# Kernel optimization log

Hardware: AMD Instinct MI355X
Metric: run time of the kernel (lower is better)

The kernel has to match this reference:

```python
import jax, jax.numpy as jnp
import numpy as np

N = 4096          # total atoms
N_METAL = 1024    # first N_METAL atoms are metal (Z=79) by construction
L = 24.0          # cubic cell edge (Angstrom)
DL = 2.4
NK = 10           # int(L / DL) -- static k-grid extent per axis
SIGMA = 1.0 / 1.805132
SCALING = 1.0
FOUR_PI = 4.0 * np.pi

# static integer reciprocal grid with k=0 removed: (K,3), K = (2*NK+1)^3 - 1
_g = np.arange(-NK, NK + 1)
_INTS = np.stack(np.meshgrid(_g, _g, _g, indexing="ij"), axis=-1).reshape(-1, 3)
_INTS = _INTS[np.any(_INTS != 0, axis=1)].astype(np.float32)


def _ewald_potential(r, q, cell):
    """Reciprocal-space Ewald potential at each atom position.
    r: (n,3) positions, q: (n,m) charges (m charge columns), cell: (3,3)
    rows = lattice vectors. Returns (n,m) potential ('field' f in cace).
    pot_i = (4*pi/V) * sum_k exp(-sigma^2 k^2/2)/k^2 * Re[S(k) e^{-ik.r_i}]."""
    recip = (2.0 * np.pi) * jnp.linalg.inv(cell).T      # rows b1,b2,b3
    k = jnp.asarray(_INTS, dtype=r.dtype) @ recip       # (K,3)
    k2 = jnp.sum(k * k, axis=1)                         # (K,)
    kfac = jnp.exp((-0.5 * SIGMA * SIGMA) * k2) / k2    # (K,)
    vol = jnp.abs(jnp.linalg.det(cell))
    kr = r @ k.T                                        # (n,K)  dominant alloc
    c, s = jnp.cos(kr), jnp.sin(kr)
    sf_c = c.T @ q                                      # (K,m) structure factors
    sf_s = s.T @ q
    pot = c @ (kfac[:, None] * sf_c) + s @ (kfac[:, None] * sf_s)
    return (FOUR_PI / vol) * pot


def setup_inputs() -> dict:
    key = jax.random.key(0)
    k1, k2 = jax.random.split(key)
    positions = jax.random.uniform(k1, (N, 3), dtype=jnp.float32) * L
    q = jax.random.normal(k2, (N, 1), dtype=jnp.float32) * 0.1
    cell = (L * jnp.eye(3, dtype=jnp.float32)).reshape(1, 3, 3)
    atomic_numbers = jnp.concatenate([
        jnp.full((N_METAL,), 79, dtype=jnp.int32),   # metal block first
        jnp.full((N - N_METAL,), 8, dtype=jnp.int32),
    ])
    batch = jnp.zeros((N,), dtype=jnp.int32)         # single system
    return {"positions": positions, "q": q, "cell": cell,
            "atomic_numbers": atomic_numbers, "batch": batch}


def reference(positions, q, cell, atomic_numbers, batch):
    # single batch (batch all zeros); metal atoms are the first N_METAL
    # (atomic_numbers == 79 by construction, so the boolean mask is static)
    cell0 = cell.reshape(3, 3)
    q = q.at[:N_METAL].set(0.0)                      # q_all[metal] = 0
    r_m = positions[:N_METAL]

    # _compute_S_matrix: pairwise Ewald kernel among metal atoms via q=eye
    A = _ewald_potential(r_m, jnp.eye(N_METAL, dtype=positions.dtype), cell0)
    coeffs = jnp.ones((N_METAL + 1, N_METAL + 1), dtype=positions.dtype)
    coeffs = coeffs.at[:N_METAL, :N_METAL].set(A)
    coeffs = coeffs.at[N_METAL, N_METAL].set(0.0)
    S = jnp.linalg.inv(coeffs)                       # cached AJl in torch code

    # field at every atom from all (electrolyte) charges
    f = _ewald_potential(positions, q, cell0)        # (N,1)

    # external_field is None -> B_ext = 0, no external energy
    B = -f[:N_METAL] * SCALING                       # (N_METAL,1)
    chi = jnp.concatenate([B, jnp.zeros((1, 1), dtype=B.dtype)], axis=0)
    sol = S @ chi                                    # (N_METAL+1,1)
    q_mw = q.at[:N_METAL].set(sol[:-1] / SCALING)
    return q_mw
```

## Files before the change

kernel.cpp:

```cpp
#include <hip/hip_runtime.h>
#include <math.h>

#define NATOM 4096
#define NM    1024
#define NKR   9260
#define KSPLIT 14
#define CHPS  22
#define NCH   308
#define KC    32
#define KPAD2 9856
#define PI_F  3.14159265358979f

typedef short v8s __attribute__((ext_vector_type(8)));
typedef float v4f __attribute__((ext_vector_type(4)));

static __device__ __forceinline__ void kdata(int t, const float* __restrict__ cell,
                                             float& kxx, float& kyy, float& kzz, float& w) {
  if (t >= NKR) { kxx = 0.f; kyy = 0.f; kzz = 0.f; w = 0.f; return; }
  int u = (t < 4630) ? t : t + 1;
  int a = u / 441;
  int rem = u - a * 441;
  int b = rem / 21;
  int c = rem - b * 21;
  float na = (float)(a - 10), nb = (float)(b - 10), nc = (float)(c - 10);
  float m00=cell[0], m01=cell[1], m02=cell[2];
  float m10=cell[3], m11=cell[4], m12=cell[5];
  float m20=cell[6], m21=cell[7], m22=cell[8];
  float det = m00*(m11*m22 - m12*m21) - m01*(m10*m22 - m12*m20) + m02*(m10*m21 - m11*m20);
  float inv00 =  (m11*m22 - m12*m21) / det;
  float inv01 = -(m01*m22 - m02*m21) / det;
  float inv02 =  (m01*m12 - m02*m11) / det;
  float inv10 = -(m10*m22 - m12*m20) / det;
  float inv11 =  (m00*m22 - m02*m20) / det;
  float inv12 = -(m00*m12 - m02*m10) / det;
  float inv20 =  (m10*m21 - m11*m20) / det;
  float inv21 = -(m00*m21 - m01*m20) / det;
  float inv22 =  (m00*m11 - m01*m10) / det;
  const float twopi = 2.f * PI_F;
  kxx = twopi * (na*inv00 + nb*inv01 + nc*inv02);
  kyy = twopi * (na*inv10 + nb*inv11 + nc*inv12);
  kzz = twopi * (na*inv20 + nb*inv21 + nc*inv22);
  float k2 = kxx*kxx + kyy*kyy + kzz*kzz;
  const float sigma = 1.0f / 1.805132f;
  w = (4.f * PI_F / fabsf(det)) * __expf(-0.5f * sigma * sigma * k2) / k2;
}

__global__ __launch_bounds__(256)
void sfk(const float* __restrict__ pos, const float* __restrict__ q,
         const float* __restrict__ cell,
         float* __restrict__ kx, float* __restrict__ ky,
         float* __restrict__ kz, float* __restrict__ ksw,
         float* __restrict__ gc, float* __restrict__ gs) {
  __shared__ float red1[8][32], red2[8][32];
  const int kloc = threadIdx.x & 31;
  const int part = threadIdx.x >> 5;
  const int k = blockIdx.x * 32 + kloc;
  float kxx, kyy, kzz, w;
  kdata(k, cell, kxx, kyy, kzz, w);
  if (part == 0) { kx[k]=kxx; ky[k]=kyy; kz[k]=kzz; ksw[k]=sqrtf(w); }
  float sc = 0.f, ss = 0.f;
  const int j0 = NM + part * 384, j1 = j0 + 384;
  for (int j = j0; j < j1; ++j) {
    float kr = kxx*pos[3*j] + kyy*pos[3*j+1] + kzz*pos[3*j+2];
    float s, c;
    __sincosf(kr, &s, &c);
    float qj = q[j];
    sc += qj * c;
    ss += qj * s;
  }
  red1[part][kloc] = sc;
  red2[part][kloc] = ss;
  __syncthreads();
  if (part == 0) {
    float tc = 0.f, ts = 0.f;
    #pragma unroll
    for (int pp = 0; pp < 8; ++pp) { tc += red1[pp][kloc]; ts += red2[pp][kloc]; }
    gc[k] = w * tc;
    gs[k] = w * ts;
  }
}

__global__ __launch_bounds__(256)
void fB(const float* __restrict__ pos,
        const float* __restrict__ kx, const float* __restrict__ ky,
        const float* __restrict__ kz,
        const float* __restrict__ gc, const float* __restrict__ gs,
        float* __restrict__ r1, float* __restrict__ r2) {
  int i = blockIdx.x;
  float px = pos[3*i], py = pos[3*i+1], pz = pos[3*i+2];
  float p = 0.f;
  for (int k = threadIdx.x; k < KPAD2; k += 256) {
    float kr = kx[k]*px + ky[k]*py + kz[k]*pz;
    float s, c;
    __sincosf(kr, &s, &c);
    p += gc[k]*c + gs[k]*s;
  }
  for (int o = 32; o > 0; o >>= 1) p += __shfl_down(p, o, 64);
  __shared__ float red[4];
  if ((threadIdx.x & 63) == 0) red[threadIdx.x >> 6] = p;
  __syncthreads();
  if (threadIdx.x == 0) {
    r1[i] = -(red[0] + red[1] + red[2] + red[3]);
    r2[i] = 1.f;
  }
}

#define PSTR 40
__global__ __launch_bounds__(256, 2)
void gemmA(const float* __restrict__ pos,
           const float* __restrict__ kx, const float* __restrict__ ky,
           const float* __restrict__ kz, const float* __restrict__ ksw,
           float* __restrict__ A) {
  __shared__ short Pl[8][128 * PSTR];
  const int blk = blockIdx.x;
  const int split = blk / 36;
  const int tt = blk - split * 36;
  int bi = 0, rem = tt;
  while (rem >= 8 - bi) { rem -= 8 - bi; ++bi; }
  const int bj = bi + rem;
  const int t = threadIdx.x;
  const int side = t >> 7;
  const int a = t & 127;
  const int atom = (side ? bj : bi) * 128 + a;
  const float px = pos[3*atom], py = pos[3*atom+1], pz = pos[3*atom+2];
  short* PC_hi = &Pl[side*4+0][a*PSTR];
  short* PC_mi = &Pl[side*4+1][a*PSTR];
  short* PS_hi = &Pl[side*4+2][a*PSTR];
  short* PS_mi = &Pl[side*4+3][a*PSTR];

  const int w = t >> 6;
  const int lane = t & 63;
  const int ln15 = lane & 15;
  const int quad = lane >> 4;

  v4f acc[2][8];
  #pragma unroll
  for (int mt = 0; mt < 2; ++mt)
    #pragma unroll
    for (int nt = 0; nt < 8; ++nt) {
      v4f z = {0.f, 0.f, 0.f, 0.f};
      acc[mt][nt] = z;
    }

  for (int ch = split * CHPS; ch < split * CHPS + CHPS; ++ch) {
    const int kb = ch * KC;
    #pragma unroll
    for (int g = 0; g < 4; ++g) {
      v8s vch, vcm, vsh, vsm;
      #pragma unroll
      for (int j = 0; j < 8; ++j) {
        const int gk = kb + g*8 + j;
        float kr = kx[gk]*px + ky[gk]*py + kz[gk]*pz;
        float s, c;
        __sincosf(kr, &s, &c);
        float sw = ksw[gk];
        float cv = c * sw, sv = s * sw;
        unsigned cu = __float_as_uint(cv);
        float chf = __uint_as_float(cu & 0xffff0000u);
        unsigned cmu = __float_as_uint(cv - chf);
        unsigned su = __float_as_uint(sv);
        float shf = __uint_as_float(su & 0xffff0000u);
        unsigned smu = __float_as_uint(sv - shf);
        vch[j] = (short)(cu >> 16);
        vcm[j] = (short)(cmu >> 16);
        vsh[j] = (short)(su >> 16);
        vsm[j] = (short)(smu >> 16);
      }
      *(v8s*)&PC_hi[g*8] = vch;
      *(v8s*)&PC_mi[g*8] = vcm;
      *(v8s*)&PS_hi[g*8] = vsh;
      *(v8s*)&PS_mi[g*8] = vsm;
    }
    __syncthreads();
    v8s aCh[2], aCm[2], aSh[2], aSm[2];
    #pragma unroll
    for (int mt = 0; mt < 2; ++mt) {
      const int off = (w*32 + mt*16 + ln15) * PSTR + quad*8;
      aCh[mt] = *(const v8s*)&Pl[0][off];
      aCm[mt] = *(const v8s*)&Pl[1][off];
      aSh[mt] = *(const v8s*)&Pl[2][off];
      aSm[mt] = *(const v8s*)&Pl[3][off];
    }
    #pragma unroll
    for (int nt = 0; nt < 8; ++nt) {
      const int off = (nt*16 + ln15) * PSTR + quad*8;
      v8s bCh = *(const v8s*)&Pl[4][off];
      v8s bCm = *(const v8s*)&Pl[5][off];
      v8s bSh = *(const v8s*)&Pl[6][off];
      v8s bSm = *(const v8s*)&Pl[7][off];
      #pragma unroll
      for (int mt = 0; mt < 2; ++mt) {
        v4f d = acc[mt][nt];
        d = __builtin_amdgcn_mfma_f32_16x16x32_bf16(aCh[mt], bCh, d, 0, 0, 0);
        d = __builtin_amdgcn_mfma_f32_16x16x32_bf16(aCh[mt], bCm, d, 0, 0, 0);
        d = __builtin_amdgcn_mfma_f32_16x16x32_bf16(aCm[mt], bCh, d, 0, 0, 0);
        d = __builtin_amdgcn_mfma_f32_16x16x32_bf16(aSh[mt], bSh, d, 0, 0, 0);
        d = __builtin_amdgcn_mfma_f32_16x16x32_bf16(aSh[mt], bSm, d, 0, 0, 0);
        d = __builtin_amdgcn_mfma_f32_16x16x32_bf16(aSm[mt], bSh, d, 0, 0, 0);
        acc[mt][nt] = d;
      }
    }
    __syncthreads();
  }
  #pragma unroll
  for (int mt = 0; mt < 2; ++mt)
    #pragma unroll
    for (int nt = 0; nt < 8; ++nt)
      #pragma unroll
      for (int r = 0; r < 4; ++r) {
        const int row = bi*128 + w*32 + mt*16 + quad*4 + r;
        const int col = bj*128 + nt*16 + ln15;
        atomicAdd(&A[row*1024 + col], acc[mt][nt][r]);
      }
}

__global__ __launch_bounds__(256)
void step(float* __restrict__ A, const float* __restrict__ r1, const float* __restrict__ r2,
          float* __restrict__ ru1, float* __restrict__ ru2,
          float* __restrict__ y1g, float* __restrict__ y2g, int p) {
  __shared__ float D[32][33];
  __shared__ float T[32][33];
  __shared__ float y1s[32], y2s[32];
  const int t = threadIdx.x;
  const int nb = 32 - p;
  const int i0 = (t >> 4) * 2, j0 = (t & 15) * 2;

  if ((int)blockIdx.x >= nb) {
    int rem = blockIdx.x - nb, a = 0;
    while (rem >= a + 1) { rem -= (a + 1); ++a; }
    const int qi = p + 1 + a, qj = p + 1 + rem;
    for (int e = t; e < 1024; e += 256) {
      int r = e >> 5, c = e & 31;
      D[r][c] = A[(qi*32+r)*1024 + (p-1)*32 + c];
      T[r][c] = A[(qj*32+r)*1024 + (p-1)*32 + c];
    }
    float o[2][2];
    if (p == 1 && (qi >> 2) != (qj >> 2)) {
      #pragma unroll
      for (int ii = 0; ii < 2; ++ii)
        #pragma unroll
        for (int jj = 0; jj < 2; ++jj)
          o[ii][jj] = A[(qj*32 + j0+jj)*1024 + qi*32 + i0+ii];
    } else {
      #pragma unroll
      for (int ii = 0; ii < 2; ++ii)
        #pragma unroll
        for (int jj = 0; jj < 2; ++jj)
          o[ii][jj] = A[(qi*32+i0+ii)*1024 + qj*32 + j0+jj];
    }
    __syncthreads();
    for (int m = 0; m < 32; ++m) {
      float a0 = D[i0+0][m], a1 = D[i0+1][m];
      float b0 = T[j0+0][m], b1 = T[j0+1][m];
      o[0][0]-=a0*b0; o[0][1]-=a0*b1;
      o[1][0]-=a1*b0; o[1][1]-=a1*b1;
    }
    #pragma unroll
    for (int ii = 0; ii < 2; ++ii)
      #pragma unroll
      for (int jj = 0; jj < 2; ++jj)
        A[(qi*32+i0+ii)*1024 + qj*32 + j0+jj] = o[ii][jj];
    return;
  }

  const int b = blockIdx.x;
  const int q = p + b;
  if (p == 0) {
    for (int e = t; e < 1024; e += 256)
      D[e>>5][e&31] = A[(e>>5)*1024 + (e&31)];
    if (b > 0) {
      if (q < 4) {
        for (int e = t; e < 1024; e += 256)
          T[e>>5][e&31] = A[(q*32+(e>>5))*1024 + (e&31)];
      } else {
        for (int e = t; e < 1024; e += 256)
          T[e&31][e>>5] = A[(e>>5)*1024 + q*32 + (e&31)];
      }
    }
    __syncthreads();
  } else {
    for (int e = t; e < 1024; e += 256)
      D[e>>5][e&31] = A[(p*32+(e>>5))*1024 + (p-1)*32 + (e&31)];
    if (b > 0)
      for (int e = t; e < 1024; e += 256)
        T[e>>5][e&31] = A[(q*32+(e>>5))*1024 + (p-1)*32 + (e&31)];
    __syncthreads();
    float o1[2][2];
    #pragma unroll
    for (int ii = 0; ii < 2; ++ii)
      #pragma unroll
      for (int jj = 0; jj < 2; ++jj)
        o1[ii][jj] = A[(p*32+i0+ii)*1024 + p*32 + j0+jj];
    for (int m = 0; m < 32; ++m) {
      float a0 = D[i0+0][m], a1 = D[i0+1][m];
      float b0 = D[j0+0][m], b1 = D[j0+1][m];
      o1[0][0]-=a0*b0; o1[0][1]-=a0*b1;
      o1[1][0]-=a1*b0; o1[1][1]-=a1*b1;
    }
    float o2[2][2];
    if (b > 0) {
      if (p == 1 && (q >> 2) != 0) {
        #pragma unroll
        for (int ii = 0; ii < 2; ++ii)
          #pragma unroll
          for (int jj = 0; jj < 2; ++jj)
            o2[ii][jj] = A[(1*32 + j0+jj)*1024 + q*32 + i0+ii];
      } else {
        #pragma unroll
        for (int ii = 0; ii < 2; ++ii)
          #pragma unroll
          for (int jj = 0; jj < 2; ++jj)
            o2[ii][jj] = A[(q*32+i0+ii)*1024 + p*32 + j0+jj];
      }
      for (int m = 0; m < 32; ++m) {
        float a0 = T[i0+0][m], a1 = T[i0+1][m];
        float b0 = D[j0+0][m], b1 = D[j0+1][m];
        o2[0][0]-=a0*b0; o2[0][1]-=a0*b1;
        o2[1][0]-=a1*b0; o2[1][1]-=a1*b1;
      }
    }
    __syncthreads();
    #pragma unroll
    for (int ii = 0; ii < 2; ++ii)
      #pragma unroll
      for (int jj = 0; jj < 2; ++jj)
        D[i0+ii][j0+jj] = o1[ii][jj];
    if (b > 0) {
      #pragma unroll
      for (int ii = 0; ii < 2; ++ii)
        #pragma unroll
        for (int jj = 0; jj < 2; ++jj)
          T[i0+ii][j0+jj] = o2[ii][jj];
    }
    __syncthreads();
  }

  if (t < 32) {
    float a[32];
    #pragma unroll
    for (int m = 0; m < 32; ++m) a[m] = D[t][m];
    #pragma unroll
    for (int j = 0; j < 32; ++j) {
      float dj = __shfl(a[j], j);
      float rinv = rsqrtf(dj);
      float lj = (t == j) ? dj * rinv : a[j] * rinv;
      a[j] = lj;
      #pragma unroll
      for (int m = j + 1; m < 32; ++m)
        a[m] -= lj * __shfl(lj, m);
    }
    #pragma unroll
    for (int m = 0; m < 32; ++m) D[t][m] = a[m];
  }
  __syncthreads();
  if (b == 0) {
    for (int e = t; e < 1024; e += 256) {
      int i = e >> 5, j = e & 31;
      if (i >= j) A[(p*32+i)*1024 + p*32 + j] = D[i][j];
    }
  } else {
    if (t < 32) {
      #pragma unroll
      for (int cb = 0; cb < 2; ++cb) {
        const int cbase = cb * 16;
        float x[16];
        #pragma unroll
        for (int k = 0; k < 16; ++k) x[k] = T[t][cbase + k];
        for (int m = 0; m < cbase; ++m) {
          float tm = T[t][m];
          #pragma unroll
          for (int k = 0; k < 16; ++k)
            x[k] -= tm * D[cbase + k][m];
        }
        #pragma unroll
        for (int k = 0; k < 16; ++k) {
          float xv = x[k] * (1.0f / D[cbase + k][cbase + k]);
          x[k] = xv;
          #pragma unroll
          for (int m2 = k + 1; m2 < 16; ++m2)
            x[m2] -= xv * D[cbase + m2][cbase + k];
        }
        #pragma unroll
        for (int k = 0; k < 16; ++k) T[t][cbase + k] = x[k];
      }
    }
    __syncthreads();
    for (int e = t; e < 1024; e += 256)
      A[(q*32 + (e>>5))*1024 + p*32 + (e&31)] = T[e>>5][e&31];
  }
  __syncthreads();
  if (t < 32) {
    float v1 = r1[p*32 + t], v2 = r2[p*32 + t];
    for (int j = 0; j < 32; ++j) {
      float invd = 1.f / D[j][j];
      float Lij = D[t][j];
      float x1 = __shfl(v1, j) * invd;
      float x2 = __shfl(v2, j) * invd;
      if (t == j)      { v1 = x1; v2 = x2; }
      else if (t > j)  { v1 -= Lij * x1; v2 -= Lij * x2; }
    }
    y1s[t] = v1; y2s[t] = v2;
    if (b == 0) { y1g[p*32 + t] = v1; y2g[p*32 + t] = v2; }
  }
  __syncthreads();
  if (b > 0 && t < 32) {
    float a1 = 0.f, a2 = 0.f;
    for (int j = 0; j < 32; ++j) {
      float lv = T[t][j];
      a1 += lv * y1s[j];
      a2 += lv * y2s[j];
    }
    ru1[q*32 + t] -= a1;
    ru2[q*32 + t] -= a2;
  }
}

__global__ __launch_bounds__(1024)
void bwd_out(const float* __restrict__ A, float* __restrict__ y1g, float* __restrict__ y2g,
             const float* __restrict__ qin, float* __restrict__ out) {
  __shared__ float D[64][65];
  __shared__ float x1s[64], x2s[64];
  __shared__ float rs1[16], rs2[16];
  const int t = threadIdx.x;
  for (int p = 15; p >= 0; --p) {
    for (int e = t; e < 4096; e += 1024)
      D[e>>6][e&63] = A[(p*64 + (e>>6))*1024 + p*64 + (e&63)];
    __syncthreads();
    if (t < 64) {
      float v1 = y1g[p*64 + t], v2 = y2g[p*64 + t];
      for (int i = 63; i >= 0; --i) {
        float invd = 1.f / D[i][i];
        float x1 = __shfl(v1, i) * invd;
        float x2 = __shfl(v2, i) * invd;
        float Lim = D[i][t];
        if (t == i)      { v1 = x1; v2 = x2; }
        else if (t < i)  { v1 -= Lim * x1; v2 -= Lim * x2; }
      }
      y1g[p*64 + t] = v1; y2g[p*64 + t] = v2;
      x1s[t] = v1; x2s[t] = v2;
    }
    __syncthreads();
    for (int rr = t; rr < p*64; rr += 1024) {
      float a1 = 0.f, a2 = 0.f;
      #pragma unroll 8
      for (int jj = 0; jj < 64; ++jj) {
        float lv = A[(p*64+jj)*1024 + rr];
        a1 += lv * x1s[jj];
        a2 += lv * x2s[jj];
      }
      y1g[rr] -= a1; y2g[rr] -= a2;
    }
    __syncthreads();
  }
  float s1 = y1g[t], s2 = y2g[t];
  for (int o = 32; o > 0; o >>= 1) { s1 += __shfl_down(s1, o, 64); s2 += __shfl_down(s2, o, 64); }
  if ((t & 63) == 0) { rs1[t >> 6] = s1; rs2[t >> 6] = s2; }
  __syncthreads();
  if (t == 0) {
    float a = 0.f, bb = 0.f;
    #pragma unroll
    for (int w = 0; w < 16; ++w) { a += rs1[w]; bb += rs2[w]; }
    rs1[0] = a / bb;
  }
  __syncthreads();
  const float lam = rs1[0];
  out[t] = y1g[t] - lam * y2g[t];
  for (int e = NM + t; e < NATOM; e += 1024) out[e] = qin[e];
}

extern "C" void kernel_launch(void* const* d_in, const int* in_sizes, int n_in,
                              void* d_out, int out_size, void* d_ws, size_t ws_size,
                              hipStream_t stream) {
  const float* pos  = (const float*)d_in[0];
  const float* q    = (const float*)d_in[1];
  const float* cell = (const float*)d_in[2];
  float* out = (float*)d_out;

  float* ws  = (float*)d_ws;
  float* A   = ws;
  float* kx  = ws + 1048576;
  float* ky  = kx + KPAD2;
  float* kz  = ky + KPAD2;
  float* ksw = kz + KPAD2;
  float* gc  = ksw + KPAD2;
  float* gs  = gc + KPAD2;
  float* r1  = gs + KPAD2;
  float* r2  = r1 + 1024;
  float* y1g = r2 + 1024;
  float* y2g = y1g + 1024;

  sfk<<<NCH, 256, 0, stream>>>(pos, q, cell, kx, ky, kz, ksw, gc, gs);
  fB<<<NM, 256, 0, stream>>>(pos, kx, ky, kz, gc, gs, r1, r2);
  hipMemsetAsync(A, 0, 1024 * 1024 * sizeof(float), stream);
  gemmA<<<36 * KSPLIT, 256, 0, stream>>>(pos, kx, ky, kz, ksw, A);
  for (int p = 0; p < 32; ++p) {
    const int s = 31 - p;
    const int grid = (32 - p) + ((p >= 1) ? s * (s + 1) / 2 : 0);
    step<<<grid, 256, 0, stream>>>(A, r1, r2, r1, r2, y1g, y2g, p);
  }
  bwd_out<<<1, 1024, 0, stream>>>(A, y1g, y2g, q, out);
}
```

Measured before the change: 974.3 us.

## Split backward triangular solve into blocked solve and multi-block update kernels

The single-block backward substitution is replaced by four 256-row super-block solves. Each solve is followed by a multi-block kernel that applies the off-diagonal update to the rows above it, so the bulk of the matrix-vector work is spread across several workgroups instead of one. The cost is extra kernel launches and the diagonal solves still running on a single 256-thread block.

Result: no change. 979.7 us (+0.6%).

```diff
diff --git a/kernel.cpp b/kernel.cpp
--- a/kernel.cpp
+++ b/kernel.cpp
@@ -415,19 +415,21 @@
   }
 }
 
-__global__ __launch_bounds__(1024)
-void bwd_out(const float* __restrict__ A, float* __restrict__ y1g, float* __restrict__ y2g,
-             const float* __restrict__ qin, float* __restrict__ out) {
+__global__ __launch_bounds__(256)
+void bwd_solve(const float* __restrict__ A, float* __restrict__ y1g, float* __restrict__ y2g,
+               const float* __restrict__ qin, float* __restrict__ out, int S, int finalize) {
   __shared__ float D[64][65];
   __shared__ float x1s[64], x2s[64];
-  __shared__ float rs1[16], rs2[16];
+  __shared__ float rs1[4], rs2[4];
   const int t = threadIdx.x;
-  for (int p = 15; p >= 0; --p) {
-    for (int e = t; e < 4096; e += 1024)
-      D[e>>6][e&63] = A[(p*64 + (e>>6))*1024 + p*64 + (e&63)];
+  const int base0 = S * 256;
+  for (int j3 = 3; j3 >= 0; --j3) {
+    const int base = base0 + j3 * 64;
+    for (int e = t; e < 4096; e += 256)
+      D[e>>6][e&63] = A[(base + (e>>6))*1024 + base + (e&63)];
     __syncthreads();
     if (t < 64) {
-      float v1 = y1g[p*64 + t], v2 = y2g[p*64 + t];
+      float v1 = y1g[base + t], v2 = y2g[base + t];
       for (int i = 63; i >= 0; --i) {
         float invd = 1.f / D[i][i];
         float x1 = __shfl(v1, i) * invd;
@@ -436,36 +438,58 @@
         if (t == i)      { v1 = x1; v2 = x2; }
         else if (t < i)  { v1 -= Lim * x1; v2 -= Lim * x2; }
       }
-      y1g[p*64 + t] = v1; y2g[p*64 + t] = v2;
+      y1g[base + t] = v1; y2g[base + t] = v2;
       x1s[t] = v1; x2s[t] = v2;
     }
     __syncthreads();
-    for (int rr = t; rr < p*64; rr += 1024) {
+    const int nup = j3 * 64;
+    for (int rr = t; rr < nup; rr += 256) {
       float a1 = 0.f, a2 = 0.f;
       #pragma unroll 8
       for (int jj = 0; jj < 64; ++jj) {
-        float lv = A[(p*64+jj)*1024 + rr];
+        float lv = A[(base+jj)*1024 + base0 + rr];
         a1 += lv * x1s[jj];
         a2 += lv * x2s[jj];
       }
-      y1g[rr] -= a1; y2g[rr] -= a2;
-    }
-    __syncthreads();
-  }
-  float s1 = y1g[t], s2 = y2g[t];
-  for (int o = 32; o > 0; o >>= 1) { s1 += __shfl_down(s1, o, 64); s2 += __shfl_down(s2, o, 64); }
-  if ((t & 63) == 0) { rs1[t >> 6] = s1; rs2[t >> 6] = s2; }
-  __syncthreads();
-  if (t == 0) {
-    float a = 0.f, bb = 0.f;
-    #pragma unroll
-    for (int w = 0; w < 16; ++w) { a += rs1[w]; bb += rs2[w]; }
-    rs1[0] = a / bb;
-  }
-  __syncthreads();
-  const float lam = rs1[0];
-  out[t] = y1g[t] - lam * y2g[t];
-  for (int e = NM + t; e < NATOM; e += 1024) out[e] = qin[e];
+      y1g[base0+rr] -= a1; y2g[base0+rr] -= a2;
+    }
+    __syncthreads();
+  }
+  if (finalize) {
+    float s1 = 0.f, s2 = 0.f;
+    for (int e = t; e < 1024; e += 256) { s1 += y1g[e]; s2 += y2g[e]; }
+    for (int o = 32; o > 0; o >>= 1) { s1 += __shfl_down(s1, o, 64); s2 += __shfl_down(s2, o, 64); }
+    if ((t & 63) == 0) { rs1[t >> 6] = s1; rs2[t >> 6] = s2; }
+    __syncthreads();
+    const float lam = (rs1[0]+rs1[1]+rs1[2]+rs1[3]) / (rs2[0]+rs2[1]+rs2[2]+rs2[3]);
+    for (int e = t; e < 1024; e += 256) out[e] = y1g[e] - lam * y2g[e];
+    for (int e = NM + t; e < NATOM; e += 256) out[e] = qin[e];
+  }
+}
+
+__global__ __launch_bounds__(256)
+void bwd_upd(const float* __restrict__ A, float* __restrict__ y1g, float* __restrict__ y2g, int S) {
+  __shared__ float x1s[256], x2s[256];
+  __shared__ float p1[4][64], p2[4][64];
+  const int t = threadIdx.x;
+  const int rbase = blockIdx.x * 64;
+  const int r = t & 63;
+  const int slice = t >> 6;
+  x1s[t] = y1g[S*256 + t];
+  x2s[t] = y2g[S*256 + t];
+  __syncthreads();
+  float a1 = 0.f, a2 = 0.f;
+  for (int j = slice*64; j < slice*64 + 64; ++j) {
+    float lv = A[(S*256 + j)*1024 + rbase + r];
+    a1 += lv * x1s[j];
+    a2 += lv * x2s[j];
+  }
+  p1[slice][r] = a1; p2[slice][r] = a2;
+  __syncthreads();
+  if (t < 64) {
+    y1g[rbase + t] -= p1[0][t] + p1[1][t] + p1[2][t] + p1[3][t];
+    y2g[rbase + t] -= p2[0][t] + p2[1][t] + p2[2][t] + p2[3][t];
+  }
 }
 
 extern "C" void kernel_launch(void* const* d_in, const int* in_sizes, int n_in,
@@ -498,5 +522,8 @@
     const int grid = (32 - p) + ((p >= 1) ? s * (s + 1) / 2 : 0);
     step<<<grid, 256, 0, stream>>>(A, r1, r2, r1, r2, y1g, y2g, p);
   }
-  bwd_out<<<1, 1024, 0, stream>>>(A, y1g, y2g, q, out);
-}
+  for (int S = 3; S >= 0; --S) {
+    bwd_solve<<<1, 256, 0, stream>>>(A, y1g, y2g, q, out, S, S == 0);
+    if (S > 0) bwd_upd<<<4 * S, 256, 0, stream>>>(A, y1g, y2g, S);
+  }
+}
```
